# Kernel tuning notes

Measured on AMD Instinct MI355X. Metric: run time of the kernel, lower is better.

The kernel has to match this reference:

```python
import jax, jax.numpy as jnp
import numpy as np

N_NODES = 100000
N_EDGES = 1600000
IN_F = 512
OUT_F = 128


def setup_inputs() -> dict:
    key = jax.random.key(0)
    k1, k2, k3, k4, k5 = jax.random.split(key, 5)
    features = jax.random.normal(k1, (N_NODES, IN_F), dtype=jnp.float32)
    # xavier_uniform-like init for the [in, out] weight
    limit = float(np.sqrt(6.0 / (IN_F + OUT_F)))
    weight = jax.random.uniform(k2, (IN_F, OUT_F), dtype=jnp.float32, minval=-limit, maxval=limit)
    edge_src = jax.random.randint(k3, (N_EDGES,), 0, N_NODES, dtype=jnp.int32)
    edge_dst = jax.random.randint(k4, (N_EDGES,), 0, N_NODES, dtype=jnp.int32)
    edge_w = jax.random.uniform(k5, (N_EDGES,), dtype=jnp.float32)
    return {"features": features, "weight": weight, "edge_src": edge_src,
            "edge_dst": edge_dst, "edge_w": edge_w}


def reference(features, weight, edge_src, edge_dst, edge_w):
    # support = features @ W  (dense GEMM, [N, out])
    support = features @ weight
    # spmm(adj, support): adj in COO form -> gather source rows, scale by
    # edge weight, scatter-add into destination rows.
    msgs = support[edge_src] * edge_w[:, None]            # [E, out]
    out = jax.ops.segment_sum(msgs, edge_dst, num_segments=N_NODES)  # [N, out]
    return jax.nn.relu(out)
```

## Files before the change

kernel.cpp:

```cpp
#include <hip/hip_runtime.h>
#include <hip/hip_bf16.h>

#define M_N 100000
#define K_F 512
#define N_F 128
#define N_E 1600000
#define NBUK 782
#define CAP 2560
#define EPB 4096

typedef __attribute__((ext_vector_type(8))) short bf16x8;
typedef __attribute__((ext_vector_type(4))) float f32x4;

__device__ __forceinline__ unsigned short f2bf(float f) {
  unsigned u = __float_as_uint(f);
  u += 0x7FFFu + ((u >> 16) & 1u);
  return (unsigned short)(u >> 16);
}

__device__ __forceinline__ unsigned pkbf(float a, float b) {
  __hip_bfloat162 h = __float22bfloat162_rn(make_float2(a, b));
  return *(unsigned*)&h;
}

__global__ void k_wt(const float* __restrict__ w, unsigned short* __restrict__ wtb) {
  int idx = blockIdx.x * 256 + threadIdx.x;
  int k = idx >> 7, n = idx & 127;
  wtb[n * K_F + k] = f2bf(w[idx]);
}

__global__ __launch_bounds__(256, 1) void k_gemm(const float* __restrict__ A,
                       const unsigned short* __restrict__ Bt,
                       unsigned short* __restrict__ S) {
  __shared__ __align__(16) float As[3][128 * 64];
  __shared__ __align__(16) unsigned short Bs[3][128 * 64];
  const int tid = threadIdx.x;
  const int lane = tid & 63;
  const int wv = tid >> 6;
  const int lr = lane & 15, lq = lane >> 4;
  const int bm0 = blockIdx.x * 128;
  const int wrow = wv * 32;

  f32x4 acc[2][8] = {};

#define STAGE(T, BUF)                                                          \
  do {                                                                         \
    _Pragma("unroll") for (int i = 0; i < 8; i++) {                            \
      int idx = i * 256 + tid;                                                 \
      int r = idx >> 4, c = idx & 15;                                          \
      int gr = bm0 + r; if (gr > M_N - 1) gr = M_N - 1;                        \
      const float* srcp = A + (size_t)gr * K_F + (T) * 64 + (c ^ (r & 7)) * 4; \
      __builtin_amdgcn_global_load_lds(                                        \
          (const __attribute__((address_space(1))) void*)srcp,                 \
          (__attribute__((address_space(3))) void*)&As[BUF][(i * 256 + wv * 64) * 4], \
          16, 0, 0);                                                           \
    }                                                                          \
    _Pragma("unroll") for (int i = 0; i < 4; i++) {                            \
      int idx = i * 256 + tid;                                                 \
      int n = idx >> 3, c = idx & 7;                                           \
      const unsigned short* srcb = Bt + (size_t)n * K_F + (T) * 64 + (c ^ (n & 7)) * 8; \
      __builtin_amdgcn_global_load_lds(                                        \
          (const __attribute__((address_space(1))) void*)srcb,                 \
          (__attribute__((address_space(3))) void*)&Bs[BUF][(i * 256 + wv * 64) * 8], \
          16, 0, 0);                                                           \
    }                                                                          \
  } while (0)

  STAGE(0, 0);
  STAGE(1, 1);

#pragma unroll
  for (int t = 0; t < 8; t++) {
    if (t < 7) asm volatile("s_waitcnt vmcnt(12)" ::: "memory");
    else       asm volatile("s_waitcnt vmcnt(0)" ::: "memory");
    __builtin_amdgcn_sched_barrier(0);
    __builtin_amdgcn_s_barrier();
    __builtin_amdgcn_sched_barrier(0);
    if (t < 6) {
      switch ((t + 2) % 3) {
        case 0: STAGE(t + 2, 0); break;
        case 1: STAGE(t + 2, 1); break;
        default: STAGE(t + 2, 2); break;
      }
    }
    const int cb_ = t % 3;
#pragma unroll
    for (int ks = 0; ks < 2; ks++) {
      bf16x8 pb[8];
#pragma unroll
      for (int n = 0; n < 8; n++) {
        int r = n * 16 + lr;
        int cc = (ks * 4 + lq) ^ (r & 7);
        pb[n] = *(const bf16x8*)&Bs[cb_][r * 64 + cc * 8];
      }
#pragma unroll
      for (int m = 0; m < 2; m++) {
        int R = wrow + m * 16 + lr;
        int cb = ks * 8 + lq * 2, sw = R & 7;
        f32x4 f0 = *(const f32x4*)&As[cb_][R * 64 + ((cb) ^ sw) * 4];
        f32x4 f1 = *(const f32x4*)&As[cb_][R * 64 + ((cb + 1) ^ sw) * 4];
        uint4 u;
        u.x = pkbf(f0[0], f0[1]);
        u.y = pkbf(f0[2], f0[3]);
        u.z = pkbf(f1[0], f1[1]);
        u.w = pkbf(f1[2], f1[3]);
        bf16x8 af = *(bf16x8*)&u;
#pragma unroll
        for (int n = 0; n < 8; n++)
          acc[m][n] = __builtin_amdgcn_mfma_f32_16x16x32_bf16(af, pb[n], acc[m][n], 0, 0, 0);
      }
    }
  }
#undef STAGE

#pragma unroll
  for (int m = 0; m < 2; m++)
#pragma unroll
    for (int j = 0; j < 4; j++) {
      int gr = bm0 + wrow + m * 16 + lq * 4 + j;
      if (gr < M_N) {
#pragma unroll
        for (int n = 0; n < 8; n++)
          S[(size_t)gr * N_F + n * 16 + lr] = f2bf(acc[m][n][j]);
      }
    }
}

__global__ void k_init(int* __restrict__ gcur) {
  int b = blockIdx.x * 256 + threadIdx.x;
  if (b < NBUK) gcur[b] = b * CAP;
}

__global__ __launch_bounds__(512) void k_bin(const int* __restrict__ src,
                                             const int* __restrict__ dst,
                                             const float* __restrict__ w,
                                             int* __restrict__ gcur,
                                             uint2* __restrict__ ebin) {
  __shared__ int lh[NBUK];
  __shared__ int lb[NBUK];
  const int tid = threadIdx.x;
  const int e0 = blockIdx.x * EPB;
  for (int b = tid; b < NBUK; b += 512) lh[b] = 0;
  __syncthreads();
#pragma unroll
  for (int i = 0; i < EPB / 512; i++) {
    int e = e0 + i * 512 + tid;
    if (e < N_E) atomicAdd(&lh[dst[e] >> 7], 1);
  }
  __syncthreads();
  for (int b = tid; b < NBUK; b += 512) {
    int c = lh[b];
    lb[b] = c ? atomicAdd(&gcur[b], c) : 0;
    lh[b] = 0;
  }
  __syncthreads();
#pragma unroll
  for (int i = 0; i < EPB / 512; i++) {
    int e = e0 + i * 512 + tid;
    if (e < N_E) {
      int d = dst[e];
      int bk = d >> 7;
      int rank = atomicAdd(&lh[bk], 1);
      ebin[lb[bk] + rank] =
          make_uint2(((unsigned)(d & 127) << 17) | (unsigned)src[e],
                     __float_as_uint(w[e]));
    }
  }
}

__global__ void k_scanB(const int* __restrict__ gcur, int* __restrict__ cbase) {
  __shared__ int sm[1024];
  int t = threadIdx.x;
  int v = (t < NBUK) ? (gcur[t] - t * CAP) : 0;
  sm[t] = v;
  __syncthreads();
  for (int off = 1; off < 1024; off <<= 1) {
    int x = sm[t];
    int a = (t >= off) ? sm[t - off] : 0;
    __syncthreads();
    sm[t] = x + a;
    __syncthreads();
  }
  if (t < NBUK) cbase[t] = sm[t] - v;
}

__global__ __launch_bounds__(256) void k_csr(const uint2* __restrict__ ebin,
                                             const int* __restrict__ gcur,
                                             const int* __restrict__ cbase,
                                             int2* __restrict__ eidx,
                                             int* __restrict__ rowstart) {
  __shared__ uint2 st[CAP];
  __shared__ int hist[128], excl[129], cur[128];
  const int b = blockIdx.x;
  const int t = threadIdx.x;
  const int cnt = gcur[b] - b * CAP;
  const uint2* eb = ebin + (size_t)b * CAP;

  if (t < 128) hist[t] = 0;
  __syncthreads();
  for (int i = t; i < cnt; i += 256) {
    uint2 e = eb[i];
    st[i] = e;
    atomicAdd(&hist[(e.x >> 17) & 127], 1);
  }
  __syncthreads();
  if (t < 128) excl[t + 1] = hist[t];
  if (t == 0) excl[0] = 0;
  __syncthreads();
  for (int off = 1; off < 128; off <<= 1) {
    int v = 0;
    if (t < 128) {
      v = excl[t + 1];
      if (t + 1 > off) v += excl[t + 1 - off];
    }
    __syncthreads();
    if (t < 128) excl[t + 1] = v;
    __syncthreads();
  }
  const int base = cbase[b];
  if (t < 128) {
    cur[t] = excl[t];
    int node = b * 128 + t;
    if (node <= M_N) rowstart[node] = base + excl[t];
  }
  __syncthreads();
  for (int i = t; i < cnt; i += 256) {
    uint2 e = st[i];
    int dl = (e.x >> 17) & 127;
    int r = atomicAdd(&cur[dl], 1);
    eidx[base + r] = make_int2((int)(e.x & 0x1FFFFu), (int)e.y);
  }
}

__device__ __forceinline__ void fma8(float* acc, float wgt, uint4 v) {
  acc[0] = fmaf(wgt, __uint_as_float(v.x << 16), acc[0]);
  acc[1] = fmaf(wgt, __uint_as_float(v.x & 0xFFFF0000u), acc[1]);
  acc[2] = fmaf(wgt, __uint_as_float(v.y << 16), acc[2]);
  acc[3] = fmaf(wgt, __uint_as_float(v.y & 0xFFFF0000u), acc[3]);
  acc[4] = fmaf(wgt, __uint_as_float(v.z << 16), acc[4]);
  acc[5] = fmaf(wgt, __uint_as_float(v.z & 0xFFFF0000u), acc[5]);
  acc[6] = fmaf(wgt, __uint_as_float(v.w << 16), acc[6]);
  acc[7] = fmaf(wgt, __uint_as_float(v.w & 0xFFFF0000u), acc[7]);
}

__global__ void k_spmm(const unsigned short* __restrict__ S,
                       const int* __restrict__ rowstart,
                       const int2* __restrict__ eidx,
                       float* __restrict__ out) {
  int wid = (blockIdx.x * 256 + threadIdx.x) >> 6;
  int lane = threadIdx.x & 63;
  if (wid >= M_N) return;
  const int g = lane >> 4;
  const int l = lane & 15;
  int s = rowstart[wid], e = rowstart[wid + 1];

  float acc[8] = {0.f, 0.f, 0.f, 0.f, 0.f, 0.f, 0.f, 0.f};

  int i = s + g;
  for (; i + 12 < e; i += 16) {
    int2 p0 = eidx[i];
    int2 p1 = eidx[i + 4];
    int2 p2 = eidx[i + 8];
    int2 p3 = eidx[i + 12];
    uint4 v0 = *(const uint4*)(S + (size_t)p0.x * N_F + l * 8);
    uint4 v1 = *(const uint4*)(S + (size_t)p1.x * N_F + l * 8);
    uint4 v2 = *(const uint4*)(S + (size_t)p2.x * N_F + l * 8);
    uint4 v3 = *(const uint4*)(S + (size_t)p3.x * N_F + l * 8);
    fma8(acc, __int_as_float(p0.y), v0);
    fma8(acc, __int_as_float(p1.y), v1);
    fma8(acc, __int_as_float(p2.y), v2);
    fma8(acc, __int_as_float(p3.y), v3);
  }
  for (; i < e; i += 4) {
    int2 p = eidx[i];
    uint4 v = *(const uint4*)(S + (size_t)p.x * N_F + l * 8);
    fma8(acc, __int_as_float(p.y), v);
  }

#pragma unroll
  for (int j = 0; j < 8; j++) {
    acc[j] += __shfl_xor(acc[j], 16, 64);
    acc[j] += __shfl_xor(acc[j], 32, 64);
    acc[j] = fmaxf(acc[j], 0.f);
  }

  if (g < 2) {
    float4 r = make_float4(acc[g * 4 + 0], acc[g * 4 + 1], acc[g * 4 + 2], acc[g * 4 + 3]);
    *(float4*)(out + (size_t)wid * N_F + l * 8 + g * 4) = r;
  }
}

extern "C" void kernel_launch(void* const* d_in, const int* in_sizes, int n_in,
                              void* d_out, int out_size, void* d_ws, size_t ws_size,
                              hipStream_t stream) {
  const float* features = (const float*)d_in[0];
  const float* weight   = (const float*)d_in[1];
  const int* edge_src   = (const int*)d_in[2];
  const int* edge_dst   = (const int*)d_in[3];
  const float* edge_w   = (const float*)d_in[4];
  float* out = (float*)d_out;

  char* ws = (char*)d_ws;
  size_t off = 0;
  unsigned short* support = (unsigned short*)(ws + off); off += (size_t)M_N * N_F * 2;
  unsigned short* wtb     = (unsigned short*)(ws + off); off += (size_t)N_F * K_F * 2;
  int* gcur     = (int*)(ws + off); off += 4096;
  int* cbase    = (int*)(ws + off); off += 4096;
  int* rowstart = (int*)(ws + off); off += ((size_t)(M_N + 1) * 4 + 255) / 256 * 256;
  uint2* ebin   = (uint2*)(ws + off); off += ((size_t)NBUK * CAP + 64) * 8;
  int2* eidx    = (int2*)(ws + off); off += (size_t)N_E * 8;

  k_wt<<<256, 256, 0, stream>>>(weight, wtb);
  k_gemm<<<(M_N + 127) / 128, 256, 0, stream>>>(features, wtb, support);
  k_init<<<4, 256, 0, stream>>>(gcur);
  k_bin<<<(N_E + EPB - 1) / EPB, 512, 0, stream>>>(edge_src, edge_dst, edge_w, gcur, ebin);
  k_scanB<<<1, 1024, 0, stream>>>(gcur, cbase);
  k_csr<<<NBUK, 256, 0, stream>>>(ebin, gcur, cbase, eidx, rowstart);
  k_spmm<<<(M_N * 64 + 255) / 256, 256, 0, stream>>>(support, rowstart, eidx, out);
}
```

Before: 189.8 us.

## Fuse bucket sort and SpMM into one per-bucket kernel, drop global CSR

Removes the global scan and CSR-build kernels and the separate SpMM. Each block of the new kernel sorts its bucket's edges into shared memory by local destination and then aggregates gathered support rows for its 128 nodes directly. Bucket-cursor init moves into the weight-transpose kernel, and the binning kernel handles twice as many edges per block. This cuts launches and the eidx/rowstart global round trip. In exchange the SpMM runs on only 782 blocks of 512 threads, each wave walking 16 nodes serially with less unrolling, so latency hiding may suffer.

Result: faster. 176.5 us (median of 2 runs) (-7.0%).

```diff
diff --git a/kernel.cpp b/kernel.cpp
--- a/kernel.cpp
+++ b/kernel.cpp
@@ -7,7 +7,7 @@
 #define N_E 1600000
 #define NBUK 782
 #define CAP 2560
-#define EPB 4096
+#define EPB 8192
 
 typedef __attribute__((ext_vector_type(8))) short bf16x8;
 typedef __attribute__((ext_vector_type(4))) float f32x4;
@@ -23,8 +23,10 @@
   return *(unsigned*)&h;
 }
 
-__global__ void k_wt(const float* __restrict__ w, unsigned short* __restrict__ wtb) {
+__global__ void k_wt(const float* __restrict__ w, unsigned short* __restrict__ wtb,
+                     int* __restrict__ gcur) {
   int idx = blockIdx.x * 256 + threadIdx.x;
+  if (idx < NBUK) gcur[idx] = idx * CAP;
   int k = idx >> 7, n = idx & 127;
   wtb[n * K_F + k] = f2bf(w[idx]);
 }
@@ -126,11 +128,6 @@
     }
 }
 
-__global__ void k_init(int* __restrict__ gcur) {
-  int b = blockIdx.x * 256 + threadIdx.x;
-  if (b < NBUK) gcur[b] = b * CAP;
-}
-
 __global__ __launch_bounds__(512) void k_bin(const int* __restrict__ src,
                                              const int* __restrict__ dst,
                                              const float* __restrict__ w,
@@ -168,70 +165,6 @@
   }
 }
 
-__global__ void k_scanB(const int* __restrict__ gcur, int* __restrict__ cbase) {
-  __shared__ int sm[1024];
-  int t = threadIdx.x;
-  int v = (t < NBUK) ? (gcur[t] - t * CAP) : 0;
-  sm[t] = v;
-  __syncthreads();
-  for (int off = 1; off < 1024; off <<= 1) {
-    int x = sm[t];
-    int a = (t >= off) ? sm[t - off] : 0;
-    __syncthreads();
-    sm[t] = x + a;
-    __syncthreads();
-  }
-  if (t < NBUK) cbase[t] = sm[t] - v;
-}
-
-__global__ __launch_bounds__(256) void k_csr(const uint2* __restrict__ ebin,
-                                             const int* __restrict__ gcur,
-                                             const int* __restrict__ cbase,
-                                             int2* __restrict__ eidx,
-                                             int* __restrict__ rowstart) {
-  __shared__ uint2 st[CAP];
-  __shared__ int hist[128], excl[129], cur[128];
-  const int b = blockIdx.x;
-  const int t = threadIdx.x;
-  const int cnt = gcur[b] - b * CAP;
-  const uint2* eb = ebin + (size_t)b * CAP;
-
-  if (t < 128) hist[t] = 0;
-  __syncthreads();
-  for (int i = t; i < cnt; i += 256) {
-    uint2 e = eb[i];
-    st[i] = e;
-    atomicAdd(&hist[(e.x >> 17) & 127], 1);
-  }
-  __syncthreads();
-  if (t < 128) excl[t + 1] = hist[t];
-  if (t == 0) excl[0] = 0;
-  __syncthreads();
-  for (int off = 1; off < 128; off <<= 1) {
-    int v = 0;
-    if (t < 128) {
-      v = excl[t + 1];
-      if (t + 1 > off) v += excl[t + 1 - off];
-    }
-    __syncthreads();
-    if (t < 128) excl[t + 1] = v;
-    __syncthreads();
-  }
-  const int base = cbase[b];
-  if (t < 128) {
-    cur[t] = excl[t];
-    int node = b * 128 + t;
-    if (node <= M_N) rowstart[node] = base + excl[t];
-  }
-  __syncthreads();
-  for (int i = t; i < cnt; i += 256) {
-    uint2 e = st[i];
-    int dl = (e.x >> 17) & 127;
-    int r = atomicAdd(&cur[dl], 1);
-    eidx[base + r] = make_int2((int)(e.x & 0x1FFFFu), (int)e.y);
-  }
-}
-
 __device__ __forceinline__ void fma8(float* acc, float wgt, uint4 v) {
   acc[0] = fmaf(wgt, __uint_as_float(v.x << 16), acc[0]);
   acc[1] = fmaf(wgt, __uint_as_float(v.x & 0xFFFF0000u), acc[1]);
@@ -243,50 +176,90 @@
   acc[7] = fmaf(wgt, __uint_as_float(v.w & 0xFFFF0000u), acc[7]);
 }
 
-__global__ void k_spmm(const unsigned short* __restrict__ S,
-                       const int* __restrict__ rowstart,
-                       const int2* __restrict__ eidx,
-                       float* __restrict__ out) {
-  int wid = (blockIdx.x * 256 + threadIdx.x) >> 6;
-  int lane = threadIdx.x & 63;
-  if (wid >= M_N) return;
+__global__ __launch_bounds__(512) void k_bspmm(const unsigned short* __restrict__ S,
+                                               const int* __restrict__ gcur,
+                                               const uint2* __restrict__ ebin,
+                                               float* __restrict__ out) {
+  __shared__ uint2 srt[CAP];
+  __shared__ int hist[128], excl[129], cur[128];
+  const int b = blockIdx.x;
+  const int t = threadIdx.x;
+  const int cnt = gcur[b] - b * CAP;
+  const uint2* eb = ebin + (size_t)b * CAP;
+
+  if (t < 128) hist[t] = 0;
+  __syncthreads();
+
+  uint2 er[5];
+  int have = 0;
+#pragma unroll
+  for (int j = 0; j < 5; j++) {
+    int i = j * 512 + t;
+    if (i < cnt) { er[j] = eb[i]; have = j + 1; }
+  }
+#pragma unroll
+  for (int j = 0; j < 5; j++)
+    if (j < have) atomicAdd(&hist[(er[j].x >> 17) & 127], 1);
+  __syncthreads();
+
+  if (t < 128) excl[t + 1] = hist[t];
+  if (t == 0) excl[0] = 0;
+  __syncthreads();
+  for (int off = 1; off < 128; off <<= 1) {
+    int v = 0;
+    if (t < 128) {
+      v = excl[t + 1];
+      if (t + 1 > off) v += excl[t + 1 - off];
+    }
+    __syncthreads();
+    if (t < 128) excl[t + 1] = v;
+    __syncthreads();
+  }
+  if (t < 128) cur[t] = excl[t];
+  __syncthreads();
+
+#pragma unroll
+  for (int j = 0; j < 5; j++)
+    if (j < have) {
+      int dl = (er[j].x >> 17) & 127;
+      int r = atomicAdd(&cur[dl], 1);
+      srt[r] = er[j];
+    }
+  __syncthreads();
+
+  const int lane = t & 63, wv = t >> 6;
   const int g = lane >> 4;
   const int l = lane & 15;
-  int s = rowstart[wid], e = rowstart[wid + 1];
-
-  float acc[8] = {0.f, 0.f, 0.f, 0.f, 0.f, 0.f, 0.f, 0.f};
-
-  int i = s + g;
-  for (; i + 12 < e; i += 16) {
-    int2 p0 = eidx[i];
-    int2 p1 = eidx[i + 4];
-    int2 p2 = eidx[i + 8];
-    int2 p3 = eidx[i + 12];
-    uint4 v0 = *(const uint4*)(S + (size_t)p0.x * N_F + l * 8);
-    uint4 v1 = *(const uint4*)(S + (size_t)p1.x * N_F + l * 8);
-    uint4 v2 = *(const uint4*)(S + (size_t)p2.x * N_F + l * 8);
-    uint4 v3 = *(const uint4*)(S + (size_t)p3.x * N_F + l * 8);
-    fma8(acc, __int_as_float(p0.y), v0);
-    fma8(acc, __int_as_float(p1.y), v1);
-    fma8(acc, __int_as_float(p2.y), v2);
-    fma8(acc, __int_as_float(p3.y), v3);
-  }
-  for (; i < e; i += 4) {
-    int2 p = eidx[i];
-    uint4 v = *(const uint4*)(S + (size_t)p.x * N_F + l * 8);
-    fma8(acc, __int_as_float(p.y), v);
-  }
-
-#pragma unroll
-  for (int j = 0; j < 8; j++) {
-    acc[j] += __shfl_xor(acc[j], 16, 64);
-    acc[j] += __shfl_xor(acc[j], 32, 64);
-    acc[j] = fmaxf(acc[j], 0.f);
-  }
-
-  if (g < 2) {
-    float4 r = make_float4(acc[g * 4 + 0], acc[g * 4 + 1], acc[g * 4 + 2], acc[g * 4 + 3]);
-    *(float4*)(out + (size_t)wid * N_F + l * 8 + g * 4) = r;
+  for (int nn = 0; nn < 16; nn++) {
+    const int ln = wv * 16 + nn;
+    const int s = excl[ln], e = excl[ln + 1];
+    float acc[8] = {0.f, 0.f, 0.f, 0.f, 0.f, 0.f, 0.f, 0.f};
+    int i = s + g;
+    for (; i + 4 < e; i += 8) {
+      uint2 p0 = srt[i];
+      uint2 p1 = srt[i + 4];
+      uint4 v0 = *(const uint4*)(S + (size_t)(p0.x & 0x1FFFFu) * N_F + l * 8);
+      uint4 v1 = *(const uint4*)(S + (size_t)(p1.x & 0x1FFFFu) * N_F + l * 8);
+      fma8(acc, __uint_as_float(p0.y), v0);
+      fma8(acc, __uint_as_float(p1.y), v1);
+    }
+    if (i < e) {
+      uint2 p = srt[i];
+      uint4 v = *(const uint4*)(S + (size_t)(p.x & 0x1FFFFu) * N_F + l * 8);
+      fma8(acc, __uint_as_float(p.y), v);
+    }
+#pragma unroll
+    for (int j = 0; j < 8; j++) {
+      acc[j] += __shfl_xor(acc[j], 16, 64);
+      acc[j] += __shfl_xor(acc[j], 32, 64);
+      acc[j] = fmaxf(acc[j], 0.f);
+    }
+    const int node = b * 128 + ln;
+    if (g < 2 && node < M_N) {
+      float4 r = make_float4(acc[g * 4 + 0], acc[g * 4 + 1],
+                             acc[g * 4 + 2], acc[g * 4 + 3]);
+      *(float4*)(out + (size_t)node * N_F + l * 8 + g * 4) = r;
+    }
   }
 }
 
@@ -304,17 +277,11 @@
   size_t off = 0;
   unsigned short* support = (unsigned short*)(ws + off); off += (size_t)M_N * N_F * 2;
   unsigned short* wtb     = (unsigned short*)(ws + off); off += (size_t)N_F * K_F * 2;
-  int* gcur     = (int*)(ws + off); off += 4096;
-  int* cbase    = (int*)(ws + off); off += 4096;
-  int* rowstart = (int*)(ws + off); off += ((size_t)(M_N + 1) * 4 + 255) / 256 * 256;
-  uint2* ebin   = (uint2*)(ws + off); off += ((size_t)NBUK * CAP + 64) * 8;
-  int2* eidx    = (int2*)(ws + off); off += (size_t)N_E * 8;
-
-  k_wt<<<256, 256, 0, stream>>>(weight, wtb);
+  int* gcur   = (int*)(ws + off); off += 4096;
+  uint2* ebin = (uint2*)(ws + off); off += ((size_t)NBUK * CAP + 64) * 8;
+
+  k_wt<<<256, 256, 0, stream>>>(weight, wtb, gcur);
   k_gemm<<<(M_N + 127) / 128, 256, 0, stream>>>(features, wtb, support);
-  k_init<<<4, 256, 0, stream>>>(gcur);
   k_bin<<<(N_E + EPB - 1) / EPB, 512, 0, stream>>>(edge_src, edge_dst, edge_w, gcur, ebin);
-  k_scanB<<<1, 1024, 0, stream>>>(gcur, cbase);
-  k_csr<<<NBUK, 256, 0, stream>>>(ebin, gcur, cbase, eidx, rowstart);
-  k_spmm<<<(M_N * 64 + 255) / 256, 256, 0, stream>>>(support, rowstart, eidx, out);
-}
+  k_bspmm<<<NBUK, 512, 0, stream>>>(support, gcur, ebin, out);
+}
```
